# Optimization experiments

Hardware: AMD Instinct MI355X
Metric: run time of the kernel (lower is better)

Reference implementation:

```python
import jax, jax.numpy as jnp
import numpy as np

STRIDE = 16


def setup_inputs() -> dict:
    key = jax.random.key(0)
    kq, kk, kv, km = jax.random.split(key, 4)
    B, H, T, D = 2, 16, 2048, 64
    q = jax.random.normal(kq, (B, H, T, D), dtype=jnp.float32)
    k = jax.random.normal(kk, (B, H, T, D), dtype=jnp.float32)
    v = jax.random.normal(kv, (B, H, T, D), dtype=jnp.float32)
    mask = jax.random.randint(km, (B, 1, 1, T), 0, 2, dtype=jnp.int32)
    return {"q": q, "k": k, "v": v, "mask": mask}


def reference(q, k, v, mask):
    # q,k,v: (B,H,T,D); mask: (B,1,1,T_k)
    B, H, T_q, D = q.shape
    T_k = k.shape[2]
    scale = 1.0 / jnp.sqrt(jnp.float32(D))
    scores = jnp.einsum("bhqd,bhkd->bhqk", q, k) * scale
    rq = jnp.arange(T_q)[:, None]
    rk = jnp.arange(T_k)[None, :]
    stride_mask = (rk % STRIDE == 0) | (rq == rk)           # (T_q, T_k) bool
    NEG = jnp.float32(-1e9)
    scores = jnp.where(stride_mask[None, None], scores, NEG)
    scores = jnp.where(mask == 0, NEG, scores)
    attn = jax.nn.softmax(scores, axis=-1)
    out = jnp.einsum("bhqk,bhkd->bhqd", attn, v)
    return (out, attn)
```

## Files before the change

### kernel.cpp

```cpp
#include <hip/hip_runtime.h>
#include <hip/hip_bf16.h>

constexpr int B = 2, H = 16, T = 2048, D = 64;
constexpr int NS = T / 16;
constexpr int WAVES = 4, BLOCK = 256;
constexpr int CHUNKS = 32;
constexpr int ROWS_PER_BLOCK = T / CHUNKS;
constexpr int ROWS_PER_WAVE = ROWS_PER_BLOCK / WAVES;
constexpr int R = 8;
constexpr int GROUPS = ROWS_PER_WAVE / R;

__device__ __forceinline__ float rlf(float v, int l) {
    return __int_as_float(__builtin_amdgcn_readlane(__float_as_int(v), l));
}
__device__ __forceinline__ unsigned bf16rne(float f) {
    unsigned x = __float_as_uint(f);
    return (x + 0x7fffu + ((x >> 16) & 1u)) >> 16;
}
__device__ __forceinline__ float bflo(unsigned u) { return __uint_as_float(u << 16); }
__device__ __forceinline__ float bfhi(unsigned u) { return __uint_as_float(u & 0xffff0000u); }

__device__ __forceinline__ int kslot(int c, int j) {
    return c ^ (j & 15) ^ (((j >> 4) & 3) << 2);
}

__global__ __launch_bounds__(BLOCK, 4)
void strided_attn_kernel(const float* __restrict__ q,
                         const float* __restrict__ k,
                         const float* __restrict__ v,
                         const int*   __restrict__ mask,
                         float* __restrict__ out,
                         float* __restrict__ attn)
{
    __shared__ uint2    Ks2[NS][16];
    __shared__ unsigned Vp[NS / 2][64];
    __shared__ int      msk[NS];

    const int blk   = blockIdx.x;
    const int bh    = blk / CHUNKS;
    const int chunk = blk % CHUNKS;
    const int b     = bh / H;

    const float* qb = q + (size_t)bh * T * D;
    const float* kb = k + (size_t)bh * T * D;
    const float* vb = v + (size_t)bh * T * D;
    const int*   mb = mask + (size_t)b * T;

    const int tid = threadIdx.x;

    for (int i = tid; i < NS * 16; i += BLOCK) {
        const int j = i >> 4, c = i & 15;
        const float4 kv = *reinterpret_cast<const float4*>(kb + (size_t)(j * 16) * D + c * 4);
        uint2 pk;
        pk.x = bf16rne(kv.x) | (bf16rne(kv.y) << 16);
        pk.y = bf16rne(kv.z) | (bf16rne(kv.w) << 16);
        Ks2[j][kslot(c, j)] = pk;
    }
    for (int i = tid; i < (NS / 2) * 64; i += BLOCK) {
        const int j2 = i >> 6, d = i & 63;
        const float f0 = vb[(size_t)(32 * j2) * D + d];
        const float f1 = vb[(size_t)(32 * j2 + 16) * D + d];
        Vp[j2][d] = bf16rne(f0) | (bf16rne(f1) << 16);
    }
    if (tid < NS) msk[tid] = mb[tid * 16];

    const int wave = tid >> 6, lane = tid & 63;
    const int row0 = chunk * ROWS_PER_BLOCK + wave * ROWS_PER_WAVE;
    const int j0 = lane, j1 = lane + 64;
    const int xsw = (lane & 15) ^ (((lane >> 4) & 3) << 2);
    const size_t bhT = (size_t)bh * T;

    const int mvals = (lane < ROWS_PER_WAVE) ? mb[row0 + lane] : 0;

    const float4 qv0  = *reinterpret_cast<const float4*>(qb + (size_t)(row0     ) * D + lane * 4);
    const float4 qv20 = *reinterpret_cast<const float4*>(qb + (size_t)(row0 +  4) * D + lane * 4);
    const float4 qv1  = *reinterpret_cast<const float4*>(qb + (size_t)(row0 +  8) * D + lane * 4);
    const float4 qv21 = *reinterpret_cast<const float4*>(qb + (size_t)(row0 + 12) * D + lane * 4);

    __syncthreads();

    const int m0 = msk[j0], m1 = msk[j1];

    #pragma unroll 1
    for (int g = 0; g < GROUPS; ++g) {
        const int grow = row0 + g * R;

        const float4 kg  = *reinterpret_cast<const float4*>(kb + (size_t)(grow    ) * D + lane * 4);
        const float4 kg2 = *reinterpret_cast<const float4*>(kb + (size_t)(grow + 4) * D + lane * 4);
        float vdr[R];
        #pragma unroll
        for (int r = 0; r < R; ++r)
            vdr[r] = vb[(size_t)(grow + r) * D + lane];

        const float4 qsel  = (g == 0) ? qv0  : qv1;
        const float4 qsel2 = (g == 0) ? qv20 : qv21;

        float s0[R], s1[R];
        #pragma unroll
        for (int r = 0; r < R; ++r) { s0[r] = 0.f; s1[r] = 0.f; }
        #pragma unroll 4
        for (int cq = 0; cq < 16; ++cq) {
            const uint2 a0 = Ks2[j0][cq ^ xsw];
            const uint2 a1 = Ks2[j1][cq ^ xsw];
            const float k0x = bflo(a0.x), k0y = bfhi(a0.x), k0z = bflo(a0.y), k0w = bfhi(a0.y);
            const float k1x = bflo(a1.x), k1y = bfhi(a1.x), k1z = bflo(a1.y), k1w = bfhi(a1.y);
            #pragma unroll
            for (int r = 0; r < R; ++r) {
                const int src = 16 * (r & 3) + cq;
                const float qx = rlf((r < 4) ? qsel.x : qsel2.x, src);
                const float qy = rlf((r < 4) ? qsel.y : qsel2.y, src);
                const float qz = rlf((r < 4) ? qsel.z : qsel2.z, src);
                const float qw = rlf((r < 4) ? qsel.w : qsel2.w, src);
                s0[r] = fmaf(qw, k0w, fmaf(qz, k0z, fmaf(qy, k0y, fmaf(qx, k0x, s0[r]))));
                s1[r] = fmaf(qw, k1w, fmaf(qz, k1z, fmaf(qy, k1y, fmaf(qx, k1x, s1[r]))));
            }
        }

        float ds = fmaf(qsel.w, kg.w, fmaf(qsel.z, kg.z, fmaf(qsel.y, kg.y, qsel.x * kg.x)));
        ds += __shfl_xor(ds, 1, 64);
        ds += __shfl_xor(ds, 2, 64);
        ds += __shfl_xor(ds, 4, 64);
        ds += __shfl_xor(ds, 8, 64);
        const float sdv = ds * 0.125f;
        float ds2 = fmaf(qsel2.w, kg2.w, fmaf(qsel2.z, kg2.z, fmaf(qsel2.y, kg2.y, qsel2.x * kg2.x)));
        ds2 += __shfl_xor(ds2, 1, 64);
        ds2 += __shfl_xor(ds2, 2, 64);
        ds2 += __shfl_xor(ds2, 4, 64);
        ds2 += __shfl_xor(ds2, 8, 64);
        const float sdv2 = ds2 * 0.125f;

        float p0[R], p1[R], pd[R];
        #pragma unroll
        for (int r = 0; r < R; ++r) {
            float a0 = s0[r] * 0.125f, a1 = s1[r] * 0.125f;
            if (m0 == 0) a0 = -1e9f;
            if (m1 == 0) a1 = -1e9f;

            float sd = (r < 4) ? rlf(sdv, 16 * r) : rlf(sdv2, 16 * (r - 4));
            if (__builtin_amdgcn_readlane(mvals, g * R + r) == 0) sd = -1e9f;
            const bool qmod = (((g * R + r) & 15) == 0);

            const float e0 = __expf(a0);
            const float e1 = __expf(a1);
            const float ed = qmod ? 0.f : __expf(sd);
            float sum = e0 + e1;
            #pragma unroll
            for (int s = 32; s > 0; s >>= 1) sum += __shfl_xor(sum, s, 64);
            sum += ed;
            const float inv = 1.f / sum;

            p0[r] = e0 * inv;
            p1[r] = e1 * inv;
            pd[r] = ed * inv;
        }

        float acc[R];
        #pragma unroll
        for (int r = 0; r < R; ++r)
            acc[r] = pd[r] * vdr[r];

        #pragma unroll 8
        for (int j2 = 0; j2 < 32; ++j2) {
            const unsigned u = Vp[j2][lane];
            const float ve = bflo(u), vo = bfhi(u);
            #pragma unroll
            for (int r = 0; r < R; ++r)
                acc[r] = fmaf(rlf(p0[r], 2 * j2 + 1), vo,
                         fmaf(rlf(p0[r], 2 * j2), ve, acc[r]));
        }
        #pragma unroll 8
        for (int j2 = 32; j2 < 64; ++j2) {
            const unsigned u = Vp[j2][lane];
            const float ve = bflo(u), vo = bfhi(u);
            #pragma unroll
            for (int r = 0; r < R; ++r)
                acc[r] = fmaf(rlf(p1[r], 2 * (j2 - 32) + 1), vo,
                         fmaf(rlf(p1[r], 2 * (j2 - 32)), ve, acc[r]));
        }

        #pragma unroll
        for (int r = 0; r < R; ++r)
            out[(bhT + grow + r) * D + lane] = acc[r];

        #pragma unroll 1
        for (int t = 0; t < 8; ++t) {
            const int f    = t * 64 + lane;
            const int idx2 = ((t & 3) * 16) + (lane >> 2);
            #pragma unroll
            for (int r = 0; r < R; ++r) {
                const int qrow = grow + r;
                const float psrc = (t < 4) ? p0[r] : p1[r];
                const float pg   = __shfl(psrc, idx2, 64);
                float4 val = make_float4(0.f, 0.f, 0.f, 0.f);
                if ((lane & 3) == 0) val.x = pg;
                const bool qmod = (((g * R + r) & 15) == 0);
                const int  fq   = qrow >> 2;
                if (!qmod && t == (fq >> 6) && lane == (fq & 63)) {
                    const int dc = r & 3;
                    if      (dc == 0) val.x = pd[r];
                    else if (dc == 1) val.y = pd[r];
                    else if (dc == 2) val.z = pd[r];
                    else              val.w = pd[r];
                }
                *reinterpret_cast<float4*>(attn + (bhT + qrow) * (size_t)T + 4 * f) = val;
            }
        }
    }
}

extern "C" void kernel_launch(void* const* d_in, const int* in_sizes, int n_in,
                              void* d_out, int out_size, void* d_ws, size_t ws_size,
                              hipStream_t stream) {
    const float* q    = (const float*)d_in[0];
    const float* k    = (const float*)d_in[1];
    const float* v    = (const float*)d_in[2];
    const int*   mask = (const int*)d_in[3];

    float* out  = (float*)d_out;
    float* attn = out + (size_t)B * H * T * D;

    dim3 grid(B * H * CHUNKS);
    dim3 block(BLOCK);
    hipLaunchKernelGGL(strided_attn_kernel, grid, block, 0, stream,
                       q, k, v, mask, out, attn);
}
```

Measured before the change: 137.2 us.

## Switch bf16 operands to packed fp16 and use v_dot2 for QK and PV

Q, K, V and the softmax probabilities are now packed as fp16 pairs (round-toward-zero), and both the score and the PV accumulations use the packed fp16 dot2 instruction. This halves the readlane and FMA counts in the inner loops, which were replacing per-element bf16 unpacking and scalar FMAs. The attention probabilities written to the attn output now pass through fp16, so they lose precision. fp16 also has a narrower range than bf16 for the inputs.

```diff
diff --git a/kernel.cpp b/kernel.cpp
--- a/kernel.cpp
+++ b/kernel.cpp
@@ -10,15 +10,25 @@
 constexpr int R = 8;
 constexpr int GROUPS = ROWS_PER_WAVE / R;
 
-__device__ __forceinline__ float rlf(float v, int l) {
-    return __int_as_float(__builtin_amdgcn_readlane(__float_as_int(v), l));
-}
-__device__ __forceinline__ unsigned bf16rne(float f) {
-    unsigned x = __float_as_uint(f);
-    return (x + 0x7fffu + ((x >> 16) & 1u)) >> 16;
-}
-__device__ __forceinline__ float bflo(unsigned u) { return __uint_as_float(u << 16); }
-__device__ __forceinline__ float bfhi(unsigned u) { return __uint_as_float(u & 0xffff0000u); }
+typedef __fp16 h2 __attribute__((ext_vector_type(2)));
+union U2H { unsigned u; h2 h; };
+
+__device__ __forceinline__ unsigned pkh(float a, float b) {
+    U2H t; t.h = __builtin_amdgcn_cvt_pkrtz(a, b); return t.u;
+}
+__device__ __forceinline__ h2 toh2(unsigned u) { U2H t; t.u = u; return t.h; }
+
+__device__ __forceinline__ float fdot2u(unsigned a, unsigned b, float c) {
+#if __has_builtin(__builtin_amdgcn_fdot2)
+    return __builtin_amdgcn_fdot2(toh2(a), toh2(b), c, false);
+#else
+    const h2 ha = toh2(a), hb = toh2(b);
+    return fmaf((float)ha.y, (float)hb.y, fmaf((float)ha.x, (float)hb.x, c));
+#endif
+}
+__device__ __forceinline__ unsigned rlu(unsigned v, int l) {
+    return (unsigned)__builtin_amdgcn_readlane((int)v, l);
+}
 
 __device__ __forceinline__ int kslot(int c, int j) {
     return c ^ (j & 15) ^ (((j >> 4) & 3) << 2);
@@ -52,15 +62,15 @@
         const int j = i >> 4, c = i & 15;
         const float4 kv = *reinterpret_cast<const float4*>(kb + (size_t)(j * 16) * D + c * 4);
         uint2 pk;
-        pk.x = bf16rne(kv.x) | (bf16rne(kv.y) << 16);
-        pk.y = bf16rne(kv.z) | (bf16rne(kv.w) << 16);
+        pk.x = pkh(kv.x, kv.y);
+        pk.y = pkh(kv.z, kv.w);
         Ks2[j][kslot(c, j)] = pk;
     }
     for (int i = tid; i < (NS / 2) * 64; i += BLOCK) {
         const int j2 = i >> 6, d = i & 63;
         const float f0 = vb[(size_t)(32 * j2) * D + d];
         const float f1 = vb[(size_t)(32 * j2 + 16) * D + d];
-        Vp[j2][d] = bf16rne(f0) | (bf16rne(f1) << 16);
+        Vp[j2][d] = pkh(f0, f1);
     }
     if (tid < NS) msk[tid] = mb[tid * 16];
 
@@ -72,10 +82,14 @@
 
     const int mvals = (lane < ROWS_PER_WAVE) ? mb[row0 + lane] : 0;
 
-    const float4 qv0  = *reinterpret_cast<const float4*>(qb + (size_t)(row0     ) * D + lane * 4);
-    const float4 qv20 = *reinterpret_cast<const float4*>(qb + (size_t)(row0 +  4) * D + lane * 4);
-    const float4 qv1  = *reinterpret_cast<const float4*>(qb + (size_t)(row0 +  8) * D + lane * 4);
-    const float4 qv21 = *reinterpret_cast<const float4*>(qb + (size_t)(row0 + 12) * D + lane * 4);
+    const float4 qf0 = *reinterpret_cast<const float4*>(qb + (size_t)(row0     ) * D + lane * 4);
+    const float4 qf1 = *reinterpret_cast<const float4*>(qb + (size_t)(row0 +  4) * D + lane * 4);
+    const float4 qf2 = *reinterpret_cast<const float4*>(qb + (size_t)(row0 +  8) * D + lane * 4);
+    const float4 qf3 = *reinterpret_cast<const float4*>(qb + (size_t)(row0 + 12) * D + lane * 4);
+    const unsigned uqg0a0 = pkh(qf0.x, qf0.y), uqg0a1 = pkh(qf0.z, qf0.w);
+    const unsigned uqg0b0 = pkh(qf1.x, qf1.y), uqg0b1 = pkh(qf1.z, qf1.w);
+    const unsigned uqg1a0 = pkh(qf2.x, qf2.y), uqg1a1 = pkh(qf2.z, qf2.w);
+    const unsigned uqg1b0 = pkh(qf3.x, qf3.y), uqg1b1 = pkh(qf3.z, qf3.w);
 
     __syncthreads();
 
@@ -92,8 +106,10 @@
         for (int r = 0; r < R; ++r)
             vdr[r] = vb[(size_t)(grow + r) * D + lane];
 
-        const float4 qsel  = (g == 0) ? qv0  : qv1;
-        const float4 qsel2 = (g == 0) ? qv20 : qv21;
+        const unsigned uqa0 = (g == 0) ? uqg0a0 : uqg1a0;
+        const unsigned uqa1 = (g == 0) ? uqg0a1 : uqg1a1;
+        const unsigned uqb0 = (g == 0) ? uqg0b0 : uqg1b0;
+        const unsigned uqb1 = (g == 0) ? uqg0b1 : uqg1b1;
 
         float s0[R], s1[R];
         #pragma unroll
@@ -102,41 +118,41 @@
         for (int cq = 0; cq < 16; ++cq) {
             const uint2 a0 = Ks2[j0][cq ^ xsw];
             const uint2 a1 = Ks2[j1][cq ^ xsw];
-            const float k0x = bflo(a0.x), k0y = bfhi(a0.x), k0z = bflo(a0.y), k0w = bfhi(a0.y);
-            const float k1x = bflo(a1.x), k1y = bfhi(a1.x), k1z = bflo(a1.y), k1w = bfhi(a1.y);
             #pragma unroll
             for (int r = 0; r < R; ++r) {
                 const int src = 16 * (r & 3) + cq;
-                const float qx = rlf((r < 4) ? qsel.x : qsel2.x, src);
-                const float qy = rlf((r < 4) ? qsel.y : qsel2.y, src);
-                const float qz = rlf((r < 4) ? qsel.z : qsel2.z, src);
-                const float qw = rlf((r < 4) ? qsel.w : qsel2.w, src);
-                s0[r] = fmaf(qw, k0w, fmaf(qz, k0z, fmaf(qy, k0y, fmaf(qx, k0x, s0[r]))));
-                s1[r] = fmaf(qw, k1w, fmaf(qz, k1z, fmaf(qy, k1y, fmaf(qx, k1x, s1[r]))));
+                const unsigned ulo = rlu((r < 4) ? uqa0 : uqb0, src);
+                const unsigned uhi = rlu((r < 4) ? uqa1 : uqb1, src);
+                s0[r] = fdot2u(uhi, a0.y, fdot2u(ulo, a0.x, s0[r]));
+                s1[r] = fdot2u(uhi, a1.y, fdot2u(ulo, a1.x, s1[r]));
             }
         }
 
-        float ds = fmaf(qsel.w, kg.w, fmaf(qsel.z, kg.z, fmaf(qsel.y, kg.y, qsel.x * kg.x)));
+        const unsigned ukg0 = pkh(kg.x, kg.y),  ukg1 = pkh(kg.z, kg.w);
+        const unsigned ukh0 = pkh(kg2.x, kg2.y), ukh1 = pkh(kg2.z, kg2.w);
+        float ds = fdot2u(uqa1, ukg1, fdot2u(uqa0, ukg0, 0.f));
         ds += __shfl_xor(ds, 1, 64);
         ds += __shfl_xor(ds, 2, 64);
         ds += __shfl_xor(ds, 4, 64);
         ds += __shfl_xor(ds, 8, 64);
         const float sdv = ds * 0.125f;
-        float ds2 = fmaf(qsel2.w, kg2.w, fmaf(qsel2.z, kg2.z, fmaf(qsel2.y, kg2.y, qsel2.x * kg2.x)));
+        float ds2 = fdot2u(uqb1, ukh1, fdot2u(uqb0, ukh0, 0.f));
         ds2 += __shfl_xor(ds2, 1, 64);
         ds2 += __shfl_xor(ds2, 2, 64);
         ds2 += __shfl_xor(ds2, 4, 64);
         ds2 += __shfl_xor(ds2, 8, 64);
         const float sdv2 = ds2 * 0.125f;
 
-        float p0[R], p1[R], pd[R];
+        unsigned pp0[R], pp1[R];
+        float pd[R];
         #pragma unroll
         for (int r = 0; r < R; ++r) {
             float a0 = s0[r] * 0.125f, a1 = s1[r] * 0.125f;
             if (m0 == 0) a0 = -1e9f;
             if (m1 == 0) a1 = -1e9f;
 
-            float sd = (r < 4) ? rlf(sdv, 16 * r) : rlf(sdv2, 16 * (r - 4));
+            float sd = (r < 4) ? __int_as_float(__builtin_amdgcn_readlane(__float_as_int(sdv), 16 * r))
+                               : __int_as_float(__builtin_amdgcn_readlane(__float_as_int(sdv2), 16 * (r - 4)));
             if (__builtin_amdgcn_readlane(mvals, g * R + r) == 0) sd = -1e9f;
             const bool qmod = (((g * R + r) & 15) == 0);
 
@@ -149,9 +165,11 @@
             sum += ed;
             const float inv = 1.f / sum;
 
-            p0[r] = e0 * inv;
-            p1[r] = e1 * inv;
+            const float p0r = e0 * inv;
+            const float p1r = e1 * inv;
             pd[r] = ed * inv;
+            pp0[r] = pkh(__shfl(p0r, 2 * lane, 64), __shfl(p0r, 2 * lane + 1, 64));
+            pp1[r] = pkh(__shfl(p1r, 2 * lane, 64), __shfl(p1r, 2 * lane + 1, 64));
         }
 
         float acc[R];
@@ -162,20 +180,16 @@
         #pragma unroll 8
         for (int j2 = 0; j2 < 32; ++j2) {
             const unsigned u = Vp[j2][lane];
-            const float ve = bflo(u), vo = bfhi(u);
             #pragma unroll
             for (int r = 0; r < R; ++r)
-                acc[r] = fmaf(rlf(p0[r], 2 * j2 + 1), vo,
-                         fmaf(rlf(p0[r], 2 * j2), ve, acc[r]));
+                acc[r] = fdot2u(rlu(pp0[r], j2), u, acc[r]);
         }
         #pragma unroll 8
-        for (int j2 = 32; j2 < 64; ++j2) {
-            const unsigned u = Vp[j2][lane];
-            const float ve = bflo(u), vo = bfhi(u);
+        for (int j2 = 0; j2 < 32; ++j2) {
+            const unsigned u = Vp[j2 + 32][lane];
             #pragma unroll
             for (int r = 0; r < R; ++r)
-                acc[r] = fmaf(rlf(p1[r], 2 * (j2 - 32) + 1), vo,
-                         fmaf(rlf(p1[r], 2 * (j2 - 32)), ve, acc[r]));
+                acc[r] = fdot2u(rlu(pp1[r], j2), u, acc[r]);
         }
 
         #pragma unroll
@@ -189,8 +203,10 @@
             #pragma unroll
             for (int r = 0; r < R; ++r) {
                 const int qrow = grow + r;
-                const float psrc = (t < 4) ? p0[r] : p1[r];
-                const float pg   = __shfl(psrc, idx2, 64);
+                const unsigned prp = (t < 4) ? pp0[r] : pp1[r];
+                const unsigned pgp = (unsigned)__shfl((int)prp, idx2 >> 1, 64);
+                const h2 ph = toh2(pgp);
+                const float pg = (float)((idx2 & 1) ? ph.y : ph.x);
                 float4 val = make_float4(0.f, 0.f, 0.f, 0.f);
                 if ((lane & 3) == 0) val.x = pg;
                 const bool qmod = (((g * R + r) & 15) == 0);
```

Measured after the change: 137.0 us. Within noise of the previous version (-0.2%).
